# Performance work log

Hardware: AMD Instinct MI355X
Metric: run time of the kernel (lower is better)

The kernel has to match this reference:

```python
import jax, jax.numpy as jnp
import numpy as np

L, D, B, N, E, T = 3, 64, 1024, 131072, 1048576, 16
CH, HID = L * D, (L * D) // 2  # channel_dim=192, reduction=2 -> 96
BN_EPS = 1e-5


def setup_inputs() -> dict:
    key = jax.random.key(0)
    ks = jax.random.split(key, 20)
    rn = lambda k, sh, s=0.1: jax.random.normal(k, sh, jnp.float32) * s
    return {
        "query_x": rn(ks[0], (N, D), 1.0),
        "corpus_x": rn(ks[1], (N, D), 1.0),
        "query_edge_index": jax.random.randint(ks[2], (2, E), 0, N),
        "corpus_edge_index": jax.random.randint(ks[3], (2, E), 0, N),
        "query_graph_idx": jnp.sort(jax.random.randint(ks[4], (N,), 0, B)),
        "corpus_graph_idx": jnp.sort(jax.random.randint(ks[5], (N,), 0, B)),
        "gin_w1": rn(ks[6], (L, D, D)),
        "gin_b1": jnp.zeros((L, D), jnp.float32),
        "gin_w2": rn(ks[7], (L, D, D)),
        "gin_b2": jnp.zeros((L, D), jnp.float32),
        "bn_gamma": jnp.ones((L, D), jnp.float32),
        "bn_beta": jnp.zeros((L, D), jnp.float32),
        "gin_eps": jnp.zeros((L,), jnp.float32),
        "inner_w": rn(ks[8], (L, D, D)),
        "inner_b": jnp.zeros((L, D), jnp.float32),
        "outer_w": rn(ks[9], (L, D, D)),
        "outer_b": jnp.zeros((L, D), jnp.float32),
        "conv_w1": rn(ks[10], (CH, HID)),
        "conv_b1": jnp.zeros((HID,), jnp.float32),
        "conv_w2": rn(ks[11], (HID, HID)),
        "conv_b2": jnp.zeros((HID,), jnp.float32),
        "score_w1": rn(ks[12], (HID, 16)),
        "score_b1": jnp.zeros((16,), jnp.float32),
        "score_w2": rn(ks[13], (16, 1)),
        "score_b2": jnp.zeros((1,), jnp.float32),
        "ntn_w": rn(ks[14], (D, D, T), 0.05),
        "ntn_wb": rn(ks[15], (T, 2 * D), 0.05),
        "ntn_bias": jnp.zeros((T,), jnp.float32),
        "sim_w1": rn(ks[16], (T, T)),
        "sim_b1": jnp.zeros((T,), jnp.float32),
        "sim_w2": rn(ks[17], (T, 1)),
        "sim_b2": jnp.zeros((1,), jnp.float32),
        "alpha": jnp.ones((1,), jnp.float32),
        "beta": jnp.ones((1,), jnp.float32),
    }


def _encode(x, edge_index, graph_idx, p):
    """EncodingLayer: per layer GINConv -> ReLU -> inner MLP -> segment-sum pool -> outer MLP."""
    src, dst = edge_index[0], edge_index[1]
    feats = []
    for i in range(L):
        agg = jax.ops.segment_sum(x[src], dst, num_segments=N)  # neighbor sum (gather->scatter)
        h = (1.0 + p["gin_eps"][i]) * x + agg                    # GIN aggregation
        h = jax.nn.relu(h @ p["gin_w1"][i] + p["gin_b1"][i]) @ p["gin_w2"][i] + p["gin_b2"][i]
        mu = h.mean(axis=0)
        var = h.var(axis=0)
        h = (h - mu) * jax.lax.rsqrt(var + BN_EPS) * p["bn_gamma"][i] + p["bn_beta"][i]  # BatchNorm1d (train stats)
        x = jax.nn.relu(h)
        inner = jax.nn.relu(x @ p["inner_w"][i] + p["inner_b"][i])
        pooled = jax.ops.segment_sum(inner, graph_idx, num_segments=B)  # [B, D] graph pooling
        feats.append(jax.nn.relu(pooled @ p["outer_w"][i] + p["outer_b"][i]))
    return jnp.concatenate(feats, axis=1)  # [B, L*D]


def reference(query_x, corpus_x, query_edge_index, corpus_edge_index, query_graph_idx, corpus_graph_idx, gin_w1, gin_b1, gin_w2, gin_b2, bn_gamma, bn_beta, gin_eps, inner_w, inner_b, outer_w, outer_b, conv_w1, conv_b1, conv_w2, conv_b2, score_w1, score_b1, score_w2, score_b2, ntn_w, ntn_wb, ntn_bias, sim_w1, sim_b1, sim_w2, sim_b2, alpha, beta):
    p = {"gin_w1": gin_w1, "gin_b1": gin_b1, "gin_w2": gin_w2, "gin_b2": gin_b2,
         "bn_gamma": bn_gamma, "bn_beta": bn_beta, "gin_eps": gin_eps,
         "inner_w": inner_w, "inner_b": inner_b, "outer_w": outer_w, "outer_b": outer_b}
    qf = _encode(query_x, query_edge_index, query_graph_idx, p)   # [B, CH]
    cf = _encode(corpus_x, corpus_edge_index, corpus_graph_idx, p)
    # diff branch: conv_stack + score_layer
    diff = jnp.exp(-jnp.square(qf - cf))
    h = jax.nn.relu(diff @ conv_w1 + conv_b1)
    h = jnp.tanh(h @ conv_w2 + conv_b2)
    score = jax.nn.sigmoid(jax.nn.relu(h @ score_w1 + score_b1) @ score_w2 + score_b2)[:, 0]
    # NTN interaction branch on last-layer (filters[-1]) graph embeddings
    e1, e2 = qf[:, -D:], cf[:, -D:]
    scoring = jnp.einsum('bf,fgt,bg->bt', e1, ntn_w, e2)
    block = jnp.concatenate([e1, e2], axis=1) @ ntn_wb.T
    sim_rep = jax.nn.relu(scoring + block + ntn_bias)
    sim = jax.nn.sigmoid(jax.nn.relu(sim_rep @ sim_w1 + sim_b1) @ sim_w2 + sim_b2)[:, 0]
    return alpha[0] * score + beta[0] * sim  # [B]
```

## Files before the change

kernel.cpp:

```cpp
#include <hip/hip_runtime.h>
#include <hip/hip_bf16.h>

typedef __hip_bfloat16 bf16;
typedef __attribute__((ext_vector_type(8))) short short8;
typedef __attribute__((ext_vector_type(4))) float floatx4;

#define NN     131072
#define NEDGE  1048576
#define BG     1024
#define LAYERS 3
#define TG     8

__device__ __forceinline__ short f2bf_s(float f){
    union { float f; unsigned u; } x; x.f = f;
    unsigned r = x.u + 0x7fffu + ((x.u >> 16) & 1u);
    return (short)(r >> 16);
}
__device__ __forceinline__ float bf2f_s(short s){
    union { unsigned u; float f; } x; x.u = ((unsigned)(unsigned short)s) << 16;
    return x.f;
}
__device__ __forceinline__ void acc4(const unsigned short* p,
                                     float& a0, float& a1, float& a2, float& a3){
    ushort4 u = *(const ushort4*)p;
    a0 += bf2f_s((short)u.x); a1 += bf2f_s((short)u.y);
    a2 += bf2f_s((short)u.z); a3 += bf2f_s((short)u.w);
}

__global__ __launch_bounds__(256) void k_zero(int* __restrict__ cnt,
    const float* __restrict__ pooled_prev, const float* __restrict__ owp,
    const float* __restrict__ obp, float* __restrict__ feats_prev)
{
    int i = blockIdx.x*256 + threadIdx.x;
    if (i < NN) cnt[i] = 0;
    if (pooled_prev && blockIdx.x < 256) {
        int bb = i >> 6, j = i & 63;
        const float* pr = pooled_prev + bb*64;
        float a = obp[j];
        for (int k = 0; k < 64; k++) a = fmaf(pr[k], owp[k*64 + j], a);
        feats_prev[bb*192 + 128 + j] = fmaxf(a, 0.f);
    }
}

__global__ __launch_bounds__(256) void k_hist(const int* __restrict__ ei,
                                              int* __restrict__ cnt,
                                              int* __restrict__ rank)
{
    int e = blockIdx.x*256 + threadIdx.x;
    rank[e] = atomicAdd(cnt + ei[NEDGE + e], 1);
}

__global__ __launch_bounds__(256) void k_scan1(const int* __restrict__ cnt,
    int* __restrict__ rowptr, int* __restrict__ bsum)
{
    __shared__ int sd[256];
    int t = threadIdx.x;
    int base = blockIdx.x*1024 + t*4;
    int c0 = cnt[base], c1 = cnt[base+1], c2 = cnt[base+2], c3 = cnt[base+3];
    int tsum = c0 + c1 + c2 + c3;
    sd[t] = tsum;
    __syncthreads();
    for (int off = 1; off < 256; off <<= 1) {
        int v = (t >= off) ? sd[t-off] : 0;
        __syncthreads();
        sd[t] += v;
        __syncthreads();
    }
    int excl = sd[t] - tsum;
    rowptr[base]   = excl;
    rowptr[base+1] = excl + c0;
    rowptr[base+2] = excl + c0 + c1;
    rowptr[base+3] = excl + c0 + c1 + c2;
    if (t == 255) bsum[blockIdx.x] = sd[255];
}

__global__ __launch_bounds__(128) void k_scan2(const int* __restrict__ bsum,
    int* __restrict__ boff, int* __restrict__ rowptr)
{
    __shared__ int sd[128];
    int t = threadIdx.x;
    int v0 = bsum[t];
    sd[t] = v0;
    __syncthreads();
    for (int off = 1; off < 128; off <<= 1) {
        int v = (t >= off) ? sd[t-off] : 0;
        __syncthreads();
        sd[t] += v;
        __syncthreads();
    }
    boff[t] = sd[t] - v0;
    if (t == 0) rowptr[NN] = NEDGE;
}

__global__ __launch_bounds__(256) void k_scan3(int* __restrict__ rowptr,
    const int* __restrict__ boff)
{
    int i = blockIdx.x*256 + threadIdx.x;
    rowptr[i] += boff[i >> 10];
}

__global__ __launch_bounds__(256) void k_fill(const int* __restrict__ ei,
    const int* __restrict__ rowptr, const int* __restrict__ rank,
    int* __restrict__ col)
{
    int e = blockIdx.x*256 + threadIdx.x;
    int s = ei[e];
    int d = ei[NEDGE + e];
    col[rowptr[d] + rank[e]] = s;
}

__global__ __launch_bounds__(256) void k_cvt(const float* __restrict__ x,
                                             bf16* __restrict__ xh,
                                             float* __restrict__ zbuf)
{
    int i = blockIdx.x*256 + threadIdx.x;
    float4 v = ((const float4*)x)[i];
    short4 o;
    o.x = f2bf_s(v.x); o.y = f2bf_s(v.y);
    o.z = f2bf_s(v.z); o.w = f2bf_s(v.w);
    ((short4*)xh)[i] = o;
    if (i < 3*128 + 3*BG*64) zbuf[i] = 0.f;
}

__global__ __launch_bounds__(256) void k_wprep(
    const float* __restrict__ gw1, const float* __restrict__ gw2,
    const float* __restrict__ iw,
    short* __restrict__ w1h, short* __restrict__ w1l,
    short* __restrict__ w2h, short* __restrict__ w2l,
    short* __restrict__ wih, short* __restrict__ wil)
{
    int i = blockIdx.x*256 + threadIdx.x;
    if (i >= 3*LAYERS*4096) return;
    int msel = i / (LAYERS*4096);
    int rem  = i % (LAYERS*4096);
    int l = rem >> 12, idx = rem & 4095;
    int n = idx >> 6, k = idx & 63;
    const float* src = (msel==0) ? gw1 : (msel==1) ? gw2 : iw;
    float v = src[l*4096 + k*64 + n];
    short hi = f2bf_s(v);
    short lo = f2bf_s(v - bf2f_s(hi));
    short* dh = (msel==0) ? w1h : (msel==1) ? w2h : wih;
    short* dl = (msel==0) ? w1l : (msel==1) ? w2l : wil;
    dh[rem] = hi;
    dl[rem] = lo;
}

__global__ __launch_bounds__(256) void k_agg_gin(
    const bf16* __restrict__ xh,
    const int* __restrict__ rowptr, const int* __restrict__ col,
    const float* __restrict__ epsp,
    const short* __restrict__ w1h, const short* __restrict__ w1l,
    const float* __restrict__ b1,
    const short* __restrict__ w2h, const short* __restrict__ w2l,
    const float* __restrict__ b2,
    float* __restrict__ big, float* __restrict__ stats,
    const float* __restrict__ pooled_prev, const float* __restrict__ owp,
    const float* __restrict__ obp, float* __restrict__ feats, int coffp)
{
    __shared__ __align__(16) char buf[4][9472];
    __shared__ float red[2][4][64];
    int tid = threadIdx.x, wv = tid >> 6, lane = tid & 63;
    int q = lane >> 4, m = lane & 15;
    int nb = blockIdx.x*128 + wv*32;
    short* Sh = (short*)buf[wv];
    short* Sl = Sh + 2304;
    float ep = 1.0f + *epsp;

    if (pooled_prev && blockIdx.x < 256) {
        int g = blockIdx.x*256 + tid;
        int bb = g >> 6, j = g & 63;
        const float* pr = pooled_prev + bb*64;
        float a = obp[j];
        for (int k = 0; k < 64; k++) a = fmaf(pr[k], owp[k*64 + j], a);
        feats[bb*192 + coffp + j] = fmaxf(a, 0.f);
    }

    int gv = rowptr[nb + (lane < 33 ? lane : 32)];
    int fo = m * 4;
    const unsigned short* xt = (const unsigned short*)xh;

    for (int i = 0; i < 8; i++) {
        int row = i*4 + q;
        int rs = __shfl(gv, row, 64);
        int re = __shfl(gv, row+1, 64);
        float a0=0.f,a1=0.f,a2=0.f,a3=0.f;
        float e0=0.f,e1=0.f,e2=0.f,e3=0.f;
        float g0=0.f,g1=0.f,g2=0.f,g3=0.f;
        float h0=0.f,h1=0.f,h2=0.f,h3=0.f;
        int r = rs;
        for (; r + 4 <= re; r += 4) {
            int ca = col[r], cb = col[r+1], cc = col[r+2], cd = col[r+3];
            acc4(xt + (((size_t)ca) << 6) + fo, a0,a1,a2,a3);
            acc4(xt + (((size_t)cb) << 6) + fo, e0,e1,e2,e3);
            acc4(xt + (((size_t)cc) << 6) + fo, g0,g1,g2,g3);
            acc4(xt + (((size_t)cd) << 6) + fo, h0,h1,h2,h3);
        }
        for (; r < re; r++)
            acc4(xt + (((size_t)col[r]) << 6) + fo, a0,a1,a2,a3);
        a0 += e0 + g0 + h0;
        a1 += e1 + g1 + h1;
        a2 += e2 + g2 + h2;
        a3 += e3 + g3 + h3;
        ushort4 sv = *(const ushort4*)(xt + (((size_t)(nb+row)) << 6) + fo);
        a0 = fmaf(ep, bf2f_s((short)sv.x), a0);
        a1 = fmaf(ep, bf2f_s((short)sv.y), a1);
        a2 = fmaf(ep, bf2f_s((short)sv.z), a2);
        a3 = fmaf(ep, bf2f_s((short)sv.w), a3);
        short4 hh, ll;
        hh.x = f2bf_s(a0); ll.x = f2bf_s(a0 - bf2f_s(hh.x));
        hh.y = f2bf_s(a1); ll.y = f2bf_s(a1 - bf2f_s(hh.y));
        hh.z = f2bf_s(a2); ll.z = f2bf_s(a2 - bf2f_s(hh.z));
        hh.w = f2bf_s(a3); ll.w = f2bf_s(a3 - bf2f_s(hh.w));
        *(short4*)(Sh + row*72 + fo) = hh;
        *(short4*)(Sl + row*72 + fo) = ll;
    }
    __syncthreads();

    short8 Ah[2][2], Al[2][2];
    #pragma unroll
    for (int mc=0; mc<2; mc++)
      #pragma unroll
      for (int kc=0; kc<2; kc++){
        Ah[mc][kc] = *(const short8*)(Sh + (mc*16+m)*72 + kc*32 + q*8);
        Al[mc][kc] = *(const short8*)(Sl + (mc*16+m)*72 + kc*32 + q*8);
      }
    floatx4 acc[2][4];
    #pragma unroll
    for (int mc=0;mc<2;mc++)
      #pragma unroll
      for (int nc=0;nc<4;nc++) acc[mc][nc] = (floatx4){0.f,0.f,0.f,0.f};
    #pragma unroll
    for (int nc=0;nc<4;nc++){
      #pragma unroll
      for (int kc=0;kc<2;kc++){
        short8 bh = *(const short8*)(w1h + (nc*16+m)*64 + kc*32 + q*8);
        short8 bl = *(const short8*)(w1l + (nc*16+m)*64 + kc*32 + q*8);
        #pragma unroll
        for (int mc=0;mc<2;mc++){
          acc[mc][nc] = __builtin_amdgcn_mfma_f32_16x16x32_bf16(Ah[mc][kc], bh, acc[mc][nc],0,0,0);
          acc[mc][nc] = __builtin_amdgcn_mfma_f32_16x16x32_bf16(Al[mc][kc], bh, acc[mc][nc],0,0,0);
          acc[mc][nc] = __builtin_amdgcn_mfma_f32_16x16x32_bf16(Ah[mc][kc], bl, acc[mc][nc],0,0,0);
        }
      }
    }

    #pragma unroll
    for (int nc=0;nc<4;nc++){
      float bia = b1[nc*16+m];
      #pragma unroll
      for (int mc=0;mc<2;mc++)
        #pragma unroll
        for (int r=0;r<4;r++){
          float v = fmaxf(acc[mc][nc][r] + bia, 0.f);
          int row = mc*16 + q*4 + r, cl = nc*16 + m;
          short hb = f2bf_s(v);
          Sh[row*72+cl] = hb;
          Sl[row*72+cl] = f2bf_s(v - bf2f_s(hb));
        }
    }
    __syncthreads();

    short8 A2h[2][2], A2l[2][2];
    #pragma unroll
    for (int mc=0; mc<2; mc++)
      #pragma unroll
      for (int kc=0; kc<2; kc++){
        A2h[mc][kc] = *(const short8*)(Sh + (mc*16+m)*72 + kc*32 + q*8);
        A2l[mc][kc] = *(const short8*)(Sl + (mc*16+m)*72 + kc*32 + q*8);
      }
    floatx4 acc2[2][4];
    #pragma unroll
    for (int mc=0;mc<2;mc++)
      #pragma unroll
      for (int nc=0;nc<4;nc++) acc2[mc][nc] = (floatx4){0.f,0.f,0.f,0.f};
    #pragma unroll
    for (int nc=0;nc<4;nc++){
      #pragma unroll
      for (int kc=0;kc<2;kc++){
        short8 bh = *(const short8*)(w2h + (nc*16+m)*64 + kc*32 + q*8);
        short8 bl = *(const short8*)(w2l + (nc*16+m)*64 + kc*32 + q*8);
        #pragma unroll
        for (int mc=0;mc<2;mc++){
          acc2[mc][nc] = __builtin_amdgcn_mfma_f32_16x16x32_bf16(A2h[mc][kc], bh, acc2[mc][nc],0,0,0);
          acc2[mc][nc] = __builtin_amdgcn_mfma_f32_16x16x32_bf16(A2l[mc][kc], bh, acc2[mc][nc],0,0,0);
          acc2[mc][nc] = __builtin_amdgcn_mfma_f32_16x16x32_bf16(A2h[mc][kc], bl, acc2[mc][nc],0,0,0);
        }
      }
    }

    #pragma unroll
    for (int nc=0;nc<4;nc++){
      float bia = b2[nc*16+m];
      float s = 0.f, s2 = 0.f;
      #pragma unroll
      for (int mc=0;mc<2;mc++)
        #pragma unroll
        for (int r=0;r<4;r++){
          float v = acc2[mc][nc][r] + bia;
          big[(((size_t)(nb + mc*16 + q*4 + r)) << 6) + nc*16 + m] = v;
          s += v; s2 = fmaf(v, v, s2);
        }
      s  += __shfl_xor(s, 16, 64);  s  += __shfl_xor(s, 32, 64);
      s2 += __shfl_xor(s2,16, 64);  s2 += __shfl_xor(s2,32, 64);
      if (q == 0){ red[0][wv][nc*16+m] = s; red[1][wv][nc*16+m] = s2; }
    }
    __syncthreads();
    if (tid < 128){
      int which = tid >> 6, c = tid & 63;
      float a = red[which][0][c]+red[which][1][c]+red[which][2][c]+red[which][3][c];
      unsafeAtomicAdd(stats + which*64 + c, a);
    }
}

__global__ __launch_bounds__(256) void k_bn_inner(
    const float* __restrict__ big, const float* __restrict__ stats,
    const float* __restrict__ gam, const float* __restrict__ bet,
    const short* __restrict__ wih, const short* __restrict__ wil,
    const float* __restrict__ bi,
    bf16* __restrict__ xh,
    const int* __restrict__ gidx, float* __restrict__ pooled)
{
    __shared__ __align__(16) char buf[4][9472];
    int tid = threadIdx.x, wv = tid >> 6, lane = tid & 63;
    int q = lane >> 4, m = lane & 15;
    int nb = blockIdx.x*128 + wv*32;
    short* Sh = (short*)buf[wv];
    short* Sl = Sh + 2304;

    float mu  = stats[lane]    * (1.0f/NN);
    float ex2 = stats[64+lane] * (1.0f/NN);
    float var = ex2 - mu*mu;
    float sc  = gam[lane] * rsqrtf(var + 1e-5f);
    float sh  = bet[lane] - mu*sc;

    for (int rr = 0; rr < 32; rr++){
        float v = big[(((size_t)(nb+rr)) << 6) + lane];
        v = fmaxf(fmaf(v, sc, sh), 0.f);
        xh[(((size_t)(nb+rr)) << 6) + lane] = __float2bfloat16(v);
        short hb = f2bf_s(v);
        Sh[rr*72 + lane] = hb;
        Sl[rr*72 + lane] = f2bf_s(v - bf2f_s(hb));
    }
    __syncthreads();

    short8 A2h[2][2], A2l[2][2];
    #pragma unroll
    for (int mc=0; mc<2; mc++)
      #pragma unroll
      for (int kc=0; kc<2; kc++){
        A2h[mc][kc] = *(const short8*)(Sh + (mc*16+m)*72 + kc*32 + q*8);
        A2l[mc][kc] = *(const short8*)(Sl + (mc*16+m)*72 + kc*32 + q*8);
      }
    floatx4 acc[2][4];
    #pragma unroll
    for (int mc=0;mc<2;mc++)
      #pragma unroll
      for (int nc=0;nc<4;nc++) acc[mc][nc] = (floatx4){0.f,0.f,0.f,0.f};
    #pragma unroll
    for (int nc=0;nc<4;nc++){
      #pragma unroll
      for (int kc=0;kc<2;kc++){
        short8 bh = *(const short8*)(wih + (nc*16+m)*64 + kc*32 + q*8);
        short8 bl = *(const short8*)(wil + (nc*16+m)*64 + kc*32 + q*8);
        #pragma unroll
        for (int mc=0;mc<2;mc++){
          acc[mc][nc] = __builtin_amdgcn_mfma_f32_16x16x32_bf16(A2h[mc][kc], bh, acc[mc][nc],0,0,0);
          acc[mc][nc] = __builtin_amdgcn_mfma_f32_16x16x32_bf16(A2l[mc][kc], bh, acc[mc][nc],0,0,0);
          acc[mc][nc] = __builtin_amdgcn_mfma_f32_16x16x32_bf16(A2h[mc][kc], bl, acc[mc][nc],0,0,0);
        }
      }
    }
    __syncthreads();

    float* P = (float*)buf[wv];
    #pragma unroll
    for (int nc=0;nc<4;nc++){
      float bia = bi[nc*16+m];
      #pragma unroll
      for (int mc=0;mc<2;mc++)
        #pragma unroll
        for (int r=0;r<4;r++){
          float v = fmaxf(acc[mc][nc][r] + bia, 0.f);
          P[(mc*16 + q*4 + r)*66 + nc*16 + m] = v;
        }
    }
    __syncthreads();

    int gv = (lane < 32) ? gidx[nb + lane] : 0;
    int cur = __shfl(gv, 0, 64);
    float a = 0.f;
    for (int rr = 0; rr < 32; rr++){
        int g = __shfl(gv, rr, 64);
        if (g != cur){
            unsafeAtomicAdd(pooled + (size_t)cur*64 + lane, a);
            a = 0.f; cur = g;
        }
        a += P[rr*66 + lane];
    }
    unsafeAtomicAdd(pooled + (size_t)cur*64 + lane, a);
}

__global__ __launch_bounds__(256) void k_tail(
    const float* __restrict__ qf, const float* __restrict__ cf,
    const float* __restrict__ pooled_c2,
    const float* __restrict__ ow2, const float* __restrict__ ob2,
    const float* __restrict__ cw1, const float* __restrict__ cb1,
    const float* __restrict__ cw2, const float* __restrict__ cb2,
    const float* __restrict__ sw1, const float* __restrict__ sb1,
    const float* __restrict__ sw2, const float* __restrict__ sb2,
    const float* __restrict__ nw,  const float* __restrict__ nwb,
    const float* __restrict__ nb,
    const float* __restrict__ mw1, const float* __restrict__ mb1,
    const float* __restrict__ mw2, const float* __restrict__ mb2,
    const float* __restrict__ alpha, const float* __restrict__ beta,
    float* __restrict__ out)
{
    __shared__ float cws[192*96];
    __shared__ float diff[TG][192];
    __shared__ float e1s[TG][64], e2s[TG][64];
    __shared__ float h1s[TG][96], h2s[TG][96];
    __shared__ float s1s[TG][16], s2s[TG][16], srep[TG][16];
    __shared__ float red[16][16][TG];

    int t = threadIdx.x;
    int b0 = blockIdx.x * TG;

    {
        int b = t >> 5, o = (t & 31) * 2;
        const float* pr = pooled_c2 + (size_t)(b0 + b)*64;
        float a0 = ob2[o], a1 = ob2[o+1];
        for (int k = 0; k < 64; k++) {
            float p = pr[k];
            a0 = fmaf(p, ow2[k*64 + o], a0);
            a1 = fmaf(p, ow2[k*64 + o + 1], a1);
        }
        e2s[b][o]   = fmaxf(a0, 0.f);
        e2s[b][o+1] = fmaxf(a1, 0.f);
    }
    for (int i = t; i < 192*96; i += 256) cws[i] = cw1[i];
    __syncthreads();

    for (int i = t; i < TG*192; i += 256) {
        int b = i / 192, f = i % 192;
        float qv = qf[(b0+b)*192 + f];
        float cv = (f < 128) ? cf[(b0+b)*192 + f] : e2s[b][f-128];
        float d = qv - cv;
        diff[b][f] = __expf(-d*d);
        if (f >= 128) e1s[b][f-128] = qv;
    }
    __syncthreads();

    {
        int b = t >> 5, o = (t & 31) * 3;
        float a0 = cb1[o], a1 = cb1[o+1], a2 = cb1[o+2];
        for (int f = 0; f < 192; f++) {
            float d = diff[b][f];
            const float* w = cws + f*96 + o;
            a0 = fmaf(d, w[0], a0);
            a1 = fmaf(d, w[1], a1);
            a2 = fmaf(d, w[2], a2);
        }
        h1s[b][o] = fmaxf(a0, 0.f);
        h1s[b][o+1] = fmaxf(a1, 0.f);
        h1s[b][o+2] = fmaxf(a2, 0.f);
    }
    __syncthreads();
    for (int i = t; i < 96*96; i += 256) cws[i] = cw2[i];
    __syncthreads();
    {
        int b = t >> 5, o = (t & 31) * 3;
        float a0 = cb2[o], a1 = cb2[o+1], a2 = cb2[o+2];
        for (int f = 0; f < 96; f++) {
            float d = h1s[b][f];
            const float* w = cws + f*96 + o;
            a0 = fmaf(d, w[0], a0);
            a1 = fmaf(d, w[1], a1);
            a2 = fmaf(d, w[2], a2);
        }
        h2s[b][o] = tanhf(a0);
        h2s[b][o+1] = tanhf(a1);
        h2s[b][o+2] = tanhf(a2);
    }
    __syncthreads();
    if (t < TG*16) {
        int b = t >> 4, o = t & 15;
        float a = sb1[o];
        for (int f = 0; f < 96; f++) a = fmaf(h2s[b][f], sw1[f*16+o], a);
        s1s[b][o] = fmaxf(a, 0.f);
    }

    {
        int tt = t & 15, gq = t >> 4;
        int g0 = gq * 4;
        int lane = t & 63;
        float e1v[TG];
        #pragma unroll
        for (int b = 0; b < TG; b++) e1v[b] = e1s[b][lane];
        float v0[TG], v1[TG], v2[TG], v3[TG];
        #pragma unroll
        for (int b = 0; b < TG; b++) { v0[b]=0.f; v1[b]=0.f; v2[b]=0.f; v3[b]=0.f; }
        for (int f = 0; f < 64; f++) {
            const float* wp = nw + ((size_t)f*64 + g0)*16 + tt;
            float w0 = wp[0], w1 = wp[16], w2 = wp[32], w3 = wp[48];
            #pragma unroll
            for (int b = 0; b < TG; b++) {
                float e = __shfl(e1v[b], f, 64);
                v0[b] = fmaf(e, w0, v0[b]);
                v1[b] = fmaf(e, w1, v1[b]);
                v2[b] = fmaf(e, w2, v2[b]);
                v3[b] = fmaf(e, w3, v3[b]);
            }
        }
        #pragma unroll
        for (int b = 0; b < TG; b++) {
            float p = v0[b]*e2s[b][g0] + v1[b]*e2s[b][g0+1]
                    + v2[b]*e2s[b][g0+2] + v3[b]*e2s[b][g0+3];
            red[gq][tt][b] = p;
        }
    }
    __syncthreads();
    if (t < TG*16) {
        int b = t >> 4, tt = t & 15;
        float scv = 0.f;
        #pragma unroll
        for (int gq = 0; gq < 16; gq++) scv += red[gq][tt][b];
        float blk = nb[tt];
        for (int f = 0; f < 64; f++) blk = fmaf(e1s[b][f], nwb[tt*128 + f], blk);
        for (int f = 0; f < 64; f++) blk = fmaf(e2s[b][f], nwb[tt*128 + 64 + f], blk);
        srep[b][tt] = fmaxf(scv + blk, 0.f);
    }
    __syncthreads();
    if (t < TG*16) {
        int b = t >> 4, o = t & 15;
        float a = mb1[o];
        #pragma unroll
        for (int f = 0; f < 16; f++) a = fmaf(srep[b][f], mw1[f*16+o], a);
        s2s[b][o] = fmaxf(a, 0.f);
    }
    __syncthreads();
    if (t < TG) {
        float sco = sb2[0], sm = mb2[0];
        #pragma unroll
        for (int f = 0; f < 16; f++) {
            sco = fmaf(s1s[t][f], sw2[f], sco);
            sm  = fmaf(s2s[t][f], mw2[f], sm);
        }
        float score = 1.f / (1.f + __expf(-sco));
        float sim   = 1.f / (1.f + __expf(-sm));
        out[b0 + t] = alpha[0]*score + beta[0]*sim;
    }
}

extern "C" void kernel_launch(void* const* d_in, const int* in_sizes, int n_in,
                              void* d_out, int out_size, void* d_ws, size_t ws_size,
                              hipStream_t stream)
{
    const float* qx  = (const float*)d_in[0];
    const float* cx  = (const float*)d_in[1];
    const int*   qei = (const int*)d_in[2];
    const int*   cei = (const int*)d_in[3];
    const int*   qgi = (const int*)d_in[4];
    const int*   cgi = (const int*)d_in[5];
    const float* Wgw1 = (const float*)d_in[6];
    const float* Wgb1 = (const float*)d_in[7];
    const float* Wgw2 = (const float*)d_in[8];
    const float* Wgb2 = (const float*)d_in[9];
    const float* Wgam = (const float*)d_in[10];
    const float* Wbet = (const float*)d_in[11];
    const float* Weps = (const float*)d_in[12];
    const float* Wiw  = (const float*)d_in[13];
    const float* Wib  = (const float*)d_in[14];
    const float* Wow  = (const float*)d_in[15];
    const float* Wob  = (const float*)d_in[16];
    const float* Wcw1 = (const float*)d_in[17];
    const float* Wcb1 = (const float*)d_in[18];
    const float* Wcw2 = (const float*)d_in[19];
    const float* Wcb2 = (const float*)d_in[20];
    const float* Wsw1 = (const float*)d_in[21];
    const float* Wsb1 = (const float*)d_in[22];
    const float* Wsw2 = (const float*)d_in[23];
    const float* Wsb2 = (const float*)d_in[24];
    const float* Wnw  = (const float*)d_in[25];
    const float* Wnwb = (const float*)d_in[26];
    const float* Wnb  = (const float*)d_in[27];
    const float* Wmw1 = (const float*)d_in[28];
    const float* Wmb1 = (const float*)d_in[29];
    const float* Wmw2 = (const float*)d_in[30];
    const float* Wmb2 = (const float*)d_in[31];
    const float* Wal  = (const float*)d_in[32];
    const float* Wbe  = (const float*)d_in[33];

    float* F      = (float*)d_ws;
    float* big    = F;
    float* zbuf   = F + 8388608;
    float* stats3 = zbuf;
    float* pooled3= zbuf + 384;
    float* qf     = pooled3 + 3*BG*64;
    float* cf     = qf + 196608;
    int*   rowptr = (int*)(cf + 196608);
    int*   cnt    = rowptr + (NN + 1);
    int*   col    = cnt + NN;
    int*   bsum   = col + NEDGE;
    int*   boff   = bsum + 128;
    bf16*  xh     = (bf16*)(boff + 128);
    int*   rank   = (int*)big;
    uintptr_t wtb = (uintptr_t)(xh + (size_t)NN*64);
    wtb = (wtb + 63) & ~((uintptr_t)63);
    short* w1h = (short*)wtb;
    short* w1l = w1h + 3*4096;
    short* w2h = w1l + 3*4096;
    short* w2l = w2h + 3*4096;
    short* wih = w2l + 3*4096;
    short* wil = wih + 3*4096;

    k_wprep<<<144, 256, 0, stream>>>(Wgw1, Wgw2, Wiw, w1h, w1l, w2h, w2l, wih, wil);

    for (int side = 0; side < 2; side++) {
        const float* x0 = side ? cx  : qx;
        const int* ei   = side ? cei : qei;
        const int* gi   = side ? cgi : qgi;
        float* feats    = side ? cf  : qf;

        if (side == 0)
            k_zero<<<NN/256, 256, 0, stream>>>(cnt, nullptr, nullptr, nullptr, nullptr);
        else
            k_zero<<<NN/256, 256, 0, stream>>>(cnt, pooled3 + 2*BG*64,
                                               Wow + 2*4096, Wob + 2*64, qf);
        k_hist<<<NEDGE/256, 256, 0, stream>>>(ei, cnt, rank);
        k_scan1<<<128, 256, 0, stream>>>(cnt, rowptr, bsum);
        k_scan2<<<1, 128, 0, stream>>>(bsum, boff, rowptr);
        k_scan3<<<NN/256, 256, 0, stream>>>(rowptr, boff);
        k_fill<<<NEDGE/256, 256, 0, stream>>>(ei, rowptr, rank, col);

        k_cvt<<<NN*64/1024, 256, 0, stream>>>(x0, xh, zbuf);

        for (int l = 0; l < LAYERS; l++) {
            const float* pprev = (l == 0) ? nullptr : pooled3 + (size_t)(l-1)*BG*64;
            const float* owp   = (l == 0) ? nullptr : Wow + (l-1)*4096;
            const float* obp   = (l == 0) ? nullptr : Wob + (l-1)*64;
            k_agg_gin<<<NN/128, 256, 0, stream>>>(xh, rowptr, col, Weps + l,
                                                  w1h + l*4096, w1l + l*4096, Wgb1 + l*64,
                                                  w2h + l*4096, w2l + l*4096, Wgb2 + l*64,
                                                  big, stats3 + l*128,
                                                  pprev, owp, obp, feats, (l-1)*64);
            k_bn_inner<<<NN/128, 256, 0, stream>>>(big, stats3 + l*128,
                                                   Wgam + l*64, Wbet + l*64,
                                                   wih + l*4096, wil + l*4096,
                                                   Wib + l*64, xh, gi,
                                                   pooled3 + (size_t)l*BG*64);
        }
    }

    k_tail<<<BG/TG, 256, 0, stream>>>(qf, cf, pooled3 + 2*BG*64,
                                      Wow + 2*4096, Wob + 2*64,
                                      Wcw1, Wcb1, Wcw2, Wcb2,
                                      Wsw1, Wsb1, Wsw2, Wsb2,
                                      Wnw, Wnwb, Wnb, Wmw1, Wmb1, Wmw2, Wmb2,
                                      Wal, Wbe, (float*)d_out);
}
```

Measured before the change: 921.2 us.

## Keep GIN MLP in registers with transposed MFMA and wider per-node gathers

Result: slower. 952.6 us (+3.4%).

```diff
diff --git a/kernel.cpp b/kernel.cpp
--- a/kernel.cpp
+++ b/kernel.cpp
@@ -20,11 +20,10 @@
     union { unsigned u; float f; } x; x.u = ((unsigned)(unsigned short)s) << 16;
     return x.f;
 }
-__device__ __forceinline__ void acc4(const unsigned short* p,
-                                     float& a0, float& a1, float& a2, float& a3){
-    ushort4 u = *(const ushort4*)p;
-    a0 += bf2f_s((short)u.x); a1 += bf2f_s((short)u.y);
-    a2 += bf2f_s((short)u.z); a3 += bf2f_s((short)u.w);
+__device__ __forceinline__ void acc8(const unsigned short* p, float* a){
+    short8 u = *(const short8*)p;
+#pragma unroll
+    for (int t = 0; t < 8; t++) a[t] += bf2f_s((short)u[t]);
 }
 
 __global__ __launch_bounds__(256) void k_zero(int* __restrict__ cnt,
@@ -133,14 +132,27 @@
     if (i >= 3*LAYERS*4096) return;
     int msel = i / (LAYERS*4096);
     int rem  = i % (LAYERS*4096);
-    int l = rem >> 12, idx = rem & 4095;
-    int n = idx >> 6, k = idx & 63;
-    const float* src = (msel==0) ? gw1 : (msel==1) ? gw2 : iw;
+    int l = rem >> 12, d = rem & 4095;
+    int k, n;
+    const float* src;
+    short *dh, *dl;
+    if (msel == 0) {
+        int j = d & 7, mm = (d>>3)&15, qq = (d>>7)&3, kc = (d>>9)&1, nc = (d>>10)&3;
+        k = qq*16 + kc*8 + j;
+        n = nc*16 + mm;
+        src = gw1; dh = w1h; dl = w1l;
+    } else if (msel == 1) {
+        int j = d & 7, mm = (d>>3)&15, qq = (d>>7)&3, kc = (d>>9)&1, nc = (d>>10)&3;
+        k = (kc*2 + (j>>2))*16 + qq*4 + (j&3);
+        n = nc*16 + mm;
+        src = gw2; dh = w2h; dl = w2l;
+    } else {
+        n = d >> 6; k = d & 63;
+        src = iw; dh = wih; dl = wil;
+    }
     float v = src[l*4096 + k*64 + n];
     short hi = f2bf_s(v);
     short lo = f2bf_s(v - bf2f_s(hi));
-    short* dh = (msel==0) ? w1h : (msel==1) ? w2h : wih;
-    short* dl = (msel==0) ? w1l : (msel==1) ? w2l : wil;
     dh[rem] = hi;
     dl[rem] = lo;
 }
@@ -157,13 +169,11 @@
     const float* __restrict__ pooled_prev, const float* __restrict__ owp,
     const float* __restrict__ obp, float* __restrict__ feats, int coffp)
 {
-    __shared__ __align__(16) char buf[4][9472];
+    __shared__ float tb[4][16*67];
     __shared__ float red[2][4][64];
     int tid = threadIdx.x, wv = tid >> 6, lane = tid & 63;
     int q = lane >> 4, m = lane & 15;
     int nb = blockIdx.x*128 + wv*32;
-    short* Sh = (short*)buf[wv];
-    short* Sl = Sh + 2304;
     float ep = 1.0f + *epsp;
 
     if (pooled_prev && blockIdx.x < 256) {
@@ -176,139 +186,131 @@
     }
 
     int gv = rowptr[nb + (lane < 33 ? lane : 32)];
-    int fo = m * 4;
+    float bv1 = b1[lane], bv2 = b2[lane];
     const unsigned short* xt = (const unsigned short*)xh;
-
-    for (int i = 0; i < 8; i++) {
-        int row = i*4 + q;
-        int rs = __shfl(gv, row, 64);
-        int re = __shfl(gv, row+1, 64);
-        float a0=0.f,a1=0.f,a2=0.f,a3=0.f;
-        float e0=0.f,e1=0.f,e2=0.f,e3=0.f;
-        float g0=0.f,g1=0.f,g2=0.f,g3=0.f;
-        float h0=0.f,h1=0.f,h2=0.f,h3=0.f;
+    int fo = q * 16;
+    float* twv = tb[wv];
+
+    for (int p = 0; p < 2; p++) {
+        int node = nb + p*16 + m;
+        int rs = __shfl(gv, p*16 + m, 64);
+        int re = __shfl(gv, p*16 + m + 1, 64);
+
+        float a0[8], a1[8];
+#pragma unroll
+        for (int t = 0; t < 8; t++) { a0[t] = 0.f; a1[t] = 0.f; }
         int r = rs;
         for (; r + 4 <= re; r += 4) {
-            int ca = col[r], cb = col[r+1], cc = col[r+2], cd = col[r+3];
-            acc4(xt + (((size_t)ca) << 6) + fo, a0,a1,a2,a3);
-            acc4(xt + (((size_t)cb) << 6) + fo, e0,e1,e2,e3);
-            acc4(xt + (((size_t)cc) << 6) + fo, g0,g1,g2,g3);
-            acc4(xt + (((size_t)cd) << 6) + fo, h0,h1,h2,h3);
-        }
-        for (; r < re; r++)
-            acc4(xt + (((size_t)col[r]) << 6) + fo, a0,a1,a2,a3);
-        a0 += e0 + g0 + h0;
-        a1 += e1 + g1 + h1;
-        a2 += e2 + g2 + h2;
-        a3 += e3 + g3 + h3;
-        ushort4 sv = *(const ushort4*)(xt + (((size_t)(nb+row)) << 6) + fo);
-        a0 = fmaf(ep, bf2f_s((short)sv.x), a0);
-        a1 = fmaf(ep, bf2f_s((short)sv.y), a1);
-        a2 = fmaf(ep, bf2f_s((short)sv.z), a2);
-        a3 = fmaf(ep, bf2f_s((short)sv.w), a3);
-        short4 hh, ll;
-        hh.x = f2bf_s(a0); ll.x = f2bf_s(a0 - bf2f_s(hh.x));
-        hh.y = f2bf_s(a1); ll.y = f2bf_s(a1 - bf2f_s(hh.y));
-        hh.z = f2bf_s(a2); ll.z = f2bf_s(a2 - bf2f_s(hh.z));
-        hh.w = f2bf_s(a3); ll.w = f2bf_s(a3 - bf2f_s(hh.w));
-        *(short4*)(Sh + row*72 + fo) = hh;
-        *(short4*)(Sl + row*72 + fo) = ll;
-    }
-    __syncthreads();
-
-    short8 Ah[2][2], Al[2][2];
-    #pragma unroll
-    for (int mc=0; mc<2; mc++)
-      #pragma unroll
-      for (int kc=0; kc<2; kc++){
-        Ah[mc][kc] = *(const short8*)(Sh + (mc*16+m)*72 + kc*32 + q*8);
-        Al[mc][kc] = *(const short8*)(Sl + (mc*16+m)*72 + kc*32 + q*8);
-      }
-    floatx4 acc[2][4];
-    #pragma unroll
-    for (int mc=0;mc<2;mc++)
-      #pragma unroll
-      for (int nc=0;nc<4;nc++) acc[mc][nc] = (floatx4){0.f,0.f,0.f,0.f};
-    #pragma unroll
-    for (int nc=0;nc<4;nc++){
-      #pragma unroll
-      for (int kc=0;kc<2;kc++){
-        short8 bh = *(const short8*)(w1h + (nc*16+m)*64 + kc*32 + q*8);
-        short8 bl = *(const short8*)(w1l + (nc*16+m)*64 + kc*32 + q*8);
-        #pragma unroll
-        for (int mc=0;mc<2;mc++){
-          acc[mc][nc] = __builtin_amdgcn_mfma_f32_16x16x32_bf16(Ah[mc][kc], bh, acc[mc][nc],0,0,0);
-          acc[mc][nc] = __builtin_amdgcn_mfma_f32_16x16x32_bf16(Al[mc][kc], bh, acc[mc][nc],0,0,0);
-          acc[mc][nc] = __builtin_amdgcn_mfma_f32_16x16x32_bf16(Ah[mc][kc], bl, acc[mc][nc],0,0,0);
-        }
-      }
-    }
-
-    #pragma unroll
-    for (int nc=0;nc<4;nc++){
-      float bia = b1[nc*16+m];
-      #pragma unroll
-      for (int mc=0;mc<2;mc++)
-        #pragma unroll
-        for (int r=0;r<4;r++){
-          float v = fmaxf(acc[mc][nc][r] + bia, 0.f);
-          int row = mc*16 + q*4 + r, cl = nc*16 + m;
-          short hb = f2bf_s(v);
-          Sh[row*72+cl] = hb;
-          Sl[row*72+cl] = f2bf_s(v - bf2f_s(hb));
-        }
-    }
-    __syncthreads();
-
-    short8 A2h[2][2], A2l[2][2];
-    #pragma unroll
-    for (int mc=0; mc<2; mc++)
-      #pragma unroll
-      for (int kc=0; kc<2; kc++){
-        A2h[mc][kc] = *(const short8*)(Sh + (mc*16+m)*72 + kc*32 + q*8);
-        A2l[mc][kc] = *(const short8*)(Sl + (mc*16+m)*72 + kc*32 + q*8);
-      }
-    floatx4 acc2[2][4];
-    #pragma unroll
-    for (int mc=0;mc<2;mc++)
-      #pragma unroll
-      for (int nc=0;nc<4;nc++) acc2[mc][nc] = (floatx4){0.f,0.f,0.f,0.f};
-    #pragma unroll
-    for (int nc=0;nc<4;nc++){
-      #pragma unroll
-      for (int kc=0;kc<2;kc++){
-        short8 bh = *(const short8*)(w2h + (nc*16+m)*64 + kc*32 + q*8);
-        short8 bl = *(const short8*)(w2l + (nc*16+m)*64 + kc*32 + q*8);
-        #pragma unroll
-        for (int mc=0;mc<2;mc++){
-          acc2[mc][nc] = __builtin_amdgcn_mfma_f32_16x16x32_bf16(A2h[mc][kc], bh, acc2[mc][nc],0,0,0);
-          acc2[mc][nc] = __builtin_amdgcn_mfma_f32_16x16x32_bf16(A2l[mc][kc], bh, acc2[mc][nc],0,0,0);
-          acc2[mc][nc] = __builtin_amdgcn_mfma_f32_16x16x32_bf16(A2h[mc][kc], bl, acc2[mc][nc],0,0,0);
-        }
-      }
-    }
-
-    #pragma unroll
-    for (int nc=0;nc<4;nc++){
-      float bia = b2[nc*16+m];
-      float s = 0.f, s2 = 0.f;
-      #pragma unroll
-      for (int mc=0;mc<2;mc++)
-        #pragma unroll
-        for (int r=0;r<4;r++){
-          float v = acc2[mc][nc][r] + bia;
-          big[(((size_t)(nb + mc*16 + q*4 + r)) << 6) + nc*16 + m] = v;
-          s += v; s2 = fmaf(v, v, s2);
-        }
-      s  += __shfl_xor(s, 16, 64);  s  += __shfl_xor(s, 32, 64);
-      s2 += __shfl_xor(s2,16, 64);  s2 += __shfl_xor(s2,32, 64);
-      if (q == 0){ red[0][wv][nc*16+m] = s; red[1][wv][nc*16+m] = s2; }
-    }
-    __syncthreads();
-    if (tid < 128){
-      int which = tid >> 6, c = tid & 63;
-      float a = red[which][0][c]+red[which][1][c]+red[which][2][c]+red[which][3][c];
-      unsafeAtomicAdd(stats + which*64 + c, a);
+            int c0 = col[r], c1 = col[r+1], c2 = col[r+2], c3 = col[r+3];
+            const unsigned short* p0 = xt + (((size_t)c0) << 6) + fo;
+            const unsigned short* p1 = xt + (((size_t)c1) << 6) + fo;
+            const unsigned short* p2 = xt + (((size_t)c2) << 6) + fo;
+            const unsigned short* p3 = xt + (((size_t)c3) << 6) + fo;
+            acc8(p0, a0); acc8(p0 + 8, a1);
+            acc8(p1, a0); acc8(p1 + 8, a1);
+            acc8(p2, a0); acc8(p2 + 8, a1);
+            acc8(p3, a0); acc8(p3 + 8, a1);
+        }
+        for (; r < re; r++) {
+            const unsigned short* pp = xt + (((size_t)col[r]) << 6) + fo;
+            acc8(pp, a0); acc8(pp + 8, a1);
+        }
+        const unsigned short* sp = xt + (((size_t)node) << 6) + fo;
+        short8 s0 = *(const short8*)sp;
+        short8 s1 = *(const short8*)(sp + 8);
+#pragma unroll
+        for (int t = 0; t < 8; t++) {
+            a0[t] = fmaf(ep, bf2f_s((short)s0[t]), a0[t]);
+            a1[t] = fmaf(ep, bf2f_s((short)s1[t]), a1[t]);
+        }
+        short8 Bh0, Bl0, Bh1, Bl1;
+#pragma unroll
+        for (int t = 0; t < 8; t++) {
+            short h0 = f2bf_s(a0[t]); Bh0[t] = h0; Bl0[t] = f2bf_s(a0[t] - bf2f_s(h0));
+            short h1 = f2bf_s(a1[t]); Bh1[t] = h1; Bl1[t] = f2bf_s(a1[t] - bf2f_s(h1));
+        }
+
+        floatx4 acc1[4];
+#pragma unroll
+        for (int nc = 0; nc < 4; nc++) acc1[nc] = (floatx4){0.f,0.f,0.f,0.f};
+#pragma unroll
+        for (int nc = 0; nc < 4; nc++) {
+#pragma unroll
+            for (int kc = 0; kc < 2; kc++) {
+                int off = ((nc*2 + kc)*4 + q)*128 + m*8;
+                short8 Ah = *(const short8*)(w1h + off);
+                short8 Al = *(const short8*)(w1l + off);
+                short8 Bh = kc ? Bh1 : Bh0;
+                short8 Bl = kc ? Bl1 : Bl0;
+                acc1[nc] = __builtin_amdgcn_mfma_f32_16x16x32_bf16(Ah, Bh, acc1[nc],0,0,0);
+                acc1[nc] = __builtin_amdgcn_mfma_f32_16x16x32_bf16(Al, Bh, acc1[nc],0,0,0);
+                acc1[nc] = __builtin_amdgcn_mfma_f32_16x16x32_bf16(Ah, Bl, acc1[nc],0,0,0);
+            }
+        }
+
+        short8 C2h[2], C2l[2];
+#pragma unroll
+        for (int kc = 0; kc < 2; kc++) {
+#pragma unroll
+            for (int hf = 0; hf < 2; hf++) {
+                int nc = kc*2 + hf;
+#pragma unroll
+                for (int rr = 0; rr < 4; rr++) {
+                    float bia = __shfl(bv1, nc*16 + q*4 + rr, 64);
+                    float vv = fmaxf(acc1[nc][rr] + bia, 0.f);
+                    short h = f2bf_s(vv);
+                    C2h[kc][hf*4 + rr] = h;
+                    C2l[kc][hf*4 + rr] = f2bf_s(vv - bf2f_s(h));
+                }
+            }
+        }
+
+        floatx4 acc2[4];
+#pragma unroll
+        for (int nc = 0; nc < 4; nc++) acc2[nc] = (floatx4){0.f,0.f,0.f,0.f};
+#pragma unroll
+        for (int nc = 0; nc < 4; nc++) {
+#pragma unroll
+            for (int kc = 0; kc < 2; kc++) {
+                int off = ((nc*2 + kc)*4 + q)*128 + m*8;
+                short8 Ah = *(const short8*)(w2h + off);
+                short8 Al = *(const short8*)(w2l + off);
+                acc2[nc] = __builtin_amdgcn_mfma_f32_16x16x32_bf16(Ah, C2h[kc], acc2[nc],0,0,0);
+                acc2[nc] = __builtin_amdgcn_mfma_f32_16x16x32_bf16(Al, C2h[kc], acc2[nc],0,0,0);
+                acc2[nc] = __builtin_amdgcn_mfma_f32_16x16x32_bf16(Ah, C2l[kc], acc2[nc],0,0,0);
+            }
+        }
+
+#pragma unroll
+        for (int nc = 0; nc < 4; nc++) {
+#pragma unroll
+            for (int rr = 0; rr < 4; rr++) {
+                float bia = __shfl(bv2, nc*16 + q*4 + rr, 64);
+                float w = acc2[nc][rr] + bia;
+                twv[m*67 + nc*16 + q*4 + rr] = w;
+                float s = w, s2 = w*w;
+                s += __shfl_xor(s, 1, 64);  s2 += __shfl_xor(s2, 1, 64);
+                s += __shfl_xor(s, 2, 64);  s2 += __shfl_xor(s2, 2, 64);
+                s += __shfl_xor(s, 4, 64);  s2 += __shfl_xor(s2, 4, 64);
+                s += __shfl_xor(s, 8, 64);  s2 += __shfl_xor(s2, 8, 64);
+                if (m == 0) {
+                    int f = nc*16 + q*4 + rr;
+                    if (p == 0) { red[0][wv][f] = s;  red[1][wv][f] = s2; }
+                    else        { red[0][wv][f] += s; red[1][wv][f] += s2; }
+                }
+            }
+        }
+        int node0 = nb + p*16;
+#pragma unroll
+        for (int rr = 0; rr < 16; rr++)
+            big[(((size_t)(node0 + rr)) << 6) + lane] = twv[rr*67 + lane];
+    }
+
+    __syncthreads();
+    if (tid < 128) {
+        int which = tid >> 6, c = tid & 63;
+        float a = red[which][0][c] + red[which][1][c] + red[which][2][c] + red[which][3][c];
+        unsafeAtomicAdd(stats + which*64 + c, a);
     }
 }
 
```
